# Kernel tuning notes

Measured on AMD Instinct MI355X. Metric: run time of the kernel, lower is better.

The kernel has to match this reference:

```python
import jax, jax.numpy as jnp
import numpy as np

N_TOKENS = 16384  # b * seq_len
D_MODEL = 4096
NUM_EXPERTS = 64
TOP_K = 2
EPS = 1e-8


def setup_inputs() -> dict:
    key = jax.random.key(0)
    kx, kw = jax.random.split(key)
    x = jax.random.normal(kx, (N_TOKENS, D_MODEL), dtype=jnp.float32)
    # nn.Linear weight: [num_experts, d_model], scaled like torch default init
    W = jax.random.normal(kw, (NUM_EXPERTS, D_MODEL), dtype=jnp.float32) / jnp.sqrt(D_MODEL)
    return {"x": x, "W": W}


def reference(x, W):
    # logits: [n_tokens, num_experts]
    logits = jnp.einsum('nd,ed->ne', x, W)
    scores = jax.nn.softmax(logits, axis=-1)
    topk_scores, topk_indices = jax.lax.top_k(scores, TOP_K)
    topk_scores = topk_scores / jnp.sum(topk_scores, axis=-1, keepdims=True)
    expert_prob = jnp.mean(scores, axis=0)  # [num_experts]
    load_balancing_loss = jnp.sum(expert_prob * jnp.log(expert_prob + EPS))
    return topk_scores, topk_indices, load_balancing_loss
```

## Files before the change

kernel.cpp:

```cpp
#include <hip/hip_runtime.h>
#include <hip/hip_bf16.h>

#define NT 16384
#define DM 4096
#define NE 64
#define MB 32
#define KSPLIT 4
#define KW (DM / KSPLIT)
#define KSTEPS (KW / 32)

typedef __attribute__((ext_vector_type(8))) short bf16x8;
typedef __attribute__((ext_vector_type(4))) float f32x4;

__device__ __forceinline__ unsigned short bf16_rne(float f) {
  const unsigned u = __float_as_uint(f);
  return (unsigned short)((u + 0x7FFFu + ((u >> 16) & 1u)) >> 16);
}

__device__ __forceinline__ void split2(float fa, float fb, unsigned& hp, unsigned& lp) {
  union { __hip_bfloat162 h; unsigned u; } cv;
  cv.h = __float22bfloat162_rn(make_float2(fa, fb));
  hp = cv.u;
  const float ha = __uint_as_float(hp << 16);
  const float hb = __uint_as_float(hp & 0xFFFF0000u);
  cv.h = __float22bfloat162_rn(make_float2(fa - ha, fb - hb));
  lp = cv.u;
}

__device__ __forceinline__ void splitA(const float4& c0, const float4& c1,
                                       bf16x8& hi, bf16x8& lo) {
  union { unsigned u[4]; bf16x8 v; } H, L;
  split2(c0.x, c0.y, H.u[0], L.u[0]);
  split2(c0.z, c0.w, H.u[1], L.u[1]);
  split2(c1.x, c1.y, H.u[2], L.u[2]);
  split2(c1.z, c1.w, H.u[3], L.u[3]);
  hi = H.v; lo = L.v;
}

__global__ void w_convert(const float* __restrict__ W,
                          unsigned short* __restrict__ Whi,
                          unsigned short* __restrict__ Wlo) {
  const int id   = blockIdx.x * 256 + threadIdx.x;
  const int lane = id & 63;
  const int nt   = (id >> 6) & 3;
  const int ks   = id >> 8;
  const float* src = W + (size_t)(nt * 16 + (lane & 15)) * DM + ks * 32 + (lane >> 4) * 8;
  unsigned short h[8], l[8];
#pragma unroll
  for (int j = 0; j < 8; ++j) {
    const float f = src[j];
    h[j] = bf16_rne(f);
    l[j] = bf16_rne(f - __uint_as_float((unsigned)h[j] << 16));
  }
  uint4 ph, pl;
  ph.x = h[0] | ((unsigned)h[1] << 16); ph.y = h[2] | ((unsigned)h[3] << 16);
  ph.z = h[4] | ((unsigned)h[5] << 16); ph.w = h[6] | ((unsigned)h[7] << 16);
  pl.x = l[0] | ((unsigned)l[1] << 16); pl.y = l[2] | ((unsigned)l[3] << 16);
  pl.z = l[4] | ((unsigned)l[5] << 16); pl.w = l[6] | ((unsigned)l[7] << 16);
  *(uint4*)(Whi + (size_t)id * 8) = ph;
  *(uint4*)(Wlo + (size_t)id * 8) = pl;
}

__launch_bounds__(256, 3)
__global__ void moe_mfma(const float* __restrict__ x,
                         const unsigned short* __restrict__ Whi,
                         const unsigned short* __restrict__ Wlo,
                         float* __restrict__ out,
                         float* __restrict__ bsum) {
  __shared__ float slab[KSPLIT][8][66];
  __shared__ float esums[4][NE];

  const int tid  = threadIdx.x;
  const int lane = tid & 63;
  const int wv   = tid >> 6;
  const int wvu  = __builtin_amdgcn_readfirstlane(wv);
  const int blk  = blockIdx.x;

  const float* ap0 = x + (size_t)(blk * MB + (lane & 15)) * DM + wv * KW + (lane >> 4) * 8;
  const float* ap1 = ap0 + (size_t)16 * DM;
  const unsigned short* bh_p = Whi + (size_t)(wv * KSTEPS) * 2048 + lane * 8;
  const unsigned short* bl_p = Wlo + (size_t)(wv * KSTEPS) * 2048 + lane * 8;

  f32x4 acc[2][4];
#pragma unroll
  for (int mt = 0; mt < 2; ++mt)
#pragma unroll
    for (int nt = 0; nt < 4; ++nt) acc[mt][nt] = (f32x4){0.f, 0.f, 0.f, 0.f};

  float4 a00 = *(const float4*)(ap0);
  float4 a01 = *(const float4*)(ap0 + 4);
  float4 a10 = *(const float4*)(ap1);
  float4 a11 = *(const float4*)(ap1 + 4);
  bf16x8 bh[4], bl[4];
#pragma unroll
  for (int nt = 0; nt < 4; ++nt) {
    bh[nt] = *(const bf16x8*)(bh_p + nt * 512);
    bl[nt] = *(const bf16x8*)(bl_p + nt * 512);
  }

#pragma unroll 2
  for (int i = 0; i < KSTEPS; ++i) {
    float4 p00, p01, p10, p11;
    bf16x8 nh[4], nl[4];
    if (i + 1 < KSTEPS) {
      const int o = (i + 1) * 32;
      p00 = *(const float4*)(ap0 + o);
      p01 = *(const float4*)(ap0 + o + 4);
      p10 = *(const float4*)(ap1 + o);
      p11 = *(const float4*)(ap1 + o + 4);
      const size_t fb = (size_t)(i + 1) * 2048;
#pragma unroll
      for (int nt = 0; nt < 4; ++nt) {
        nh[nt] = *(const bf16x8*)(bh_p + fb + nt * 512);
        nl[nt] = *(const bf16x8*)(bl_p + fb + nt * 512);
      }
    }

    bf16x8 ah0, al0, ah1, al1;
    splitA(a00, a01, ah0, al0);
    splitA(a10, a11, ah1, al1);

#pragma unroll
    for (int nt = 0; nt < 4; ++nt) {
      acc[0][nt] = __builtin_amdgcn_mfma_f32_16x16x32_bf16(al0, bl[nt], acc[0][nt], 0, 0, 0);
      acc[0][nt] = __builtin_amdgcn_mfma_f32_16x16x32_bf16(al0, bh[nt], acc[0][nt], 0, 0, 0);
      acc[0][nt] = __builtin_amdgcn_mfma_f32_16x16x32_bf16(ah0, bl[nt], acc[0][nt], 0, 0, 0);
      acc[0][nt] = __builtin_amdgcn_mfma_f32_16x16x32_bf16(ah0, bh[nt], acc[0][nt], 0, 0, 0);
      acc[1][nt] = __builtin_amdgcn_mfma_f32_16x16x32_bf16(al1, bl[nt], acc[1][nt], 0, 0, 0);
      acc[1][nt] = __builtin_amdgcn_mfma_f32_16x16x32_bf16(al1, bh[nt], acc[1][nt], 0, 0, 0);
      acc[1][nt] = __builtin_amdgcn_mfma_f32_16x16x32_bf16(ah1, bl[nt], acc[1][nt], 0, 0, 0);
      acc[1][nt] = __builtin_amdgcn_mfma_f32_16x16x32_bf16(ah1, bh[nt], acc[1][nt], 0, 0, 0);
    }

    if (i + 1 < KSTEPS) {
      a00 = p00; a01 = p01; a10 = p10; a11 = p11;
#pragma unroll
      for (int nt = 0; nt < 4; ++nt) { bh[nt] = nh[nt]; bl[nt] = nl[nt]; }
    }
  }

  float lg[8];
#pragma unroll
  for (int s = 0; s < 4; ++s) {
    const int mt = s >> 1;
    const int g  = 2 * (s & 1);
    const int q  = lane >> 4;
    if (q == g || q == g + 1) {
#pragma unroll
      for (int nt = 0; nt < 4; ++nt)
#pragma unroll
        for (int r = 0; r < 4; ++r)
          slab[wv][(q - g) * 4 + r][nt * 16 + (lane & 15)] = acc[mt][nt][r];
    }
    __syncthreads();
    if (wvu == s) {
#pragma unroll
      for (int t = 0; t < 8; ++t) {
        float v = 0.f;
#pragma unroll
        for (int w = 0; w < KSPLIT; ++w) v += slab[w][t][lane];
        lg[t] = v;
      }
    }
    __syncthreads();
  }

  float esum = 0.f;
#pragma unroll
  for (int ti = 0; ti < 8; ++ti) {
    const float lgv = lg[ti];
    float m = lgv;
#pragma unroll
    for (int off = 32; off; off >>= 1) m = fmaxf(m, __shfl_xor(m, off, 64));
    const float p = __expf(lgv - m);
    float Z = p;
#pragma unroll
    for (int off = 32; off; off >>= 1) Z += __shfl_xor(Z, off, 64);
    const float s = p / Z;
    esum += s;

    float v1 = s; int i1 = lane;
#pragma unroll
    for (int off = 32; off; off >>= 1) {
      const float ov = __shfl_xor(v1, off, 64);
      const int   oi = __shfl_xor(i1, off, 64);
      if (ov > v1 || (ov == v1 && oi < i1)) { v1 = ov; i1 = oi; }
    }
    float sv = (lane == i1) ? -1.f : s;
    float v2 = sv; int i2 = lane;
#pragma unroll
    for (int off = 32; off; off >>= 1) {
      const float ov = __shfl_xor(v2, off, 64);
      const int   oi = __shfl_xor(i2, off, 64);
      if (ov > v2 || (ov == v2 && oi < i2)) { v2 = ov; i2 = oi; }
    }

    if (lane == 0) {
      const int gt = blk * MB + wvu * 8 + ti;
      const float inv = 1.f / (v1 + v2);
      out[2 * gt]              = v1 * inv;
      out[2 * gt + 1]          = v2 * inv;
      out[2 * NT + 2 * gt]     = (float)i1;
      out[2 * NT + 2 * gt + 1] = (float)i2;
    }
  }

  esums[wvu][lane] = esum;
  __syncthreads();
  if (wvu == 0) {
    float tot = esums[0][lane] + esums[1][lane] + esums[2][lane] + esums[3][lane];
    bsum[blk * NE + lane] = tot;
  }
}

__global__ void moe_gate_loss(const float* __restrict__ bsum,
                              float* __restrict__ out) {
  __shared__ float red[4][64];
  const int e = threadIdx.x & 63;
  const int g = threadIdx.x >> 6;
  float s = 0.f;
  for (int b = g; b < NT / MB; b += 4) s += bsum[b * 64 + e];
  red[g][e] = s;
  __syncthreads();
  if (threadIdx.x < 64) {
    const float tot = red[0][e] + red[1][e] + red[2][e] + red[3][e];
    const float p = tot * (1.f / (float)NT);
    float term = p * logf(p + 1e-8f);
#pragma unroll
    for (int off = 32; off; off >>= 1) term += __shfl_xor(term, off, 64);
    if (e == 0) out[4 * NT] = term;
  }
}

extern "C" void kernel_launch(void* const* d_in, const int* in_sizes, int n_in,
                              void* d_out, int out_size, void* d_ws, size_t ws_size,
                              hipStream_t stream) {
  const float* x = (const float*)d_in[0];
  const float* W = (const float*)d_in[1];
  float* out = (float*)d_out;

  unsigned short* Whi = (unsigned short*)d_ws;
  unsigned short* Wlo = Whi + (size_t)NE * DM;
  float* bsum = (float*)(Wlo + (size_t)NE * DM);

  hipLaunchKernelGGL(w_convert, dim3(128), dim3(256), 0, stream, W, Whi, Wlo);
  hipLaunchKernelGGL(moe_mfma, dim3(NT / MB), dim3(256), 0, stream, x, Whi, Wlo, out, bsum);
  hipLaunchKernelGGL(moe_gate_loss, dim3(1), dim3(256), 0, stream, bsum, out);
}
```

Measured before the change: 111.2 us.

## Stage x tiles through double-buffered LDS and drop split-K reduction

The GEMM kernel now processes 64 tokens per block with 512 threads. Each wave owns a 16-token by 32-expert tile over the full K range, instead of four waves splitting K and reducing through shared memory. Activations are staged with coalesced row loads into a double-buffered LDS tile. Bf16 hi/lo weight fragments are software-pipelined from global memory. This removes the cross-wave split-K reduction and makes x loads coalesced, at the cost of a barrier per K stage and half the grid size.

```diff
diff --git a/kernel.cpp b/kernel.cpp
--- a/kernel.cpp
+++ b/kernel.cpp
@@ -4,10 +4,10 @@
 #define NT 16384
 #define DM 4096
 #define NE 64
-#define MB 32
-#define KSPLIT 4
-#define KW (DM / KSPLIT)
-#define KSTEPS (KW / 32)
+#define MB 64
+#define BK 128
+#define NST (DM / BK)
+#define LROW 132
 
 typedef __attribute__((ext_vector_type(8))) short bf16x8;
 typedef __attribute__((ext_vector_type(4))) float f32x4;
@@ -61,114 +61,107 @@
   *(uint4*)(Wlo + (size_t)id * 8) = pl;
 }
 
-__launch_bounds__(256, 3)
+__launch_bounds__(512, 2)
 __global__ void moe_mfma(const float* __restrict__ x,
                          const unsigned short* __restrict__ Whi,
                          const unsigned short* __restrict__ Wlo,
                          float* __restrict__ out,
                          float* __restrict__ bsum) {
-  __shared__ float slab[KSPLIT][8][66];
-  __shared__ float esums[4][NE];
+  __shared__ float xs[2][MB][LROW];
+  __shared__ float esums[8][NE];
+  float* lg = &xs[0][0][0];
 
   const int tid  = threadIdx.x;
   const int lane = tid & 63;
   const int wv   = tid >> 6;
   const int wvu  = __builtin_amdgcn_readfirstlane(wv);
+  const int tg   = wvu >> 1;
+  const int eg   = wvu & 1;
   const int blk  = blockIdx.x;
-
-  const float* ap0 = x + (size_t)(blk * MB + (lane & 15)) * DM + wv * KW + (lane >> 4) * 8;
-  const float* ap1 = ap0 + (size_t)16 * DM;
-  const unsigned short* bh_p = Whi + (size_t)(wv * KSTEPS) * 2048 + lane * 8;
-  const unsigned short* bl_p = Wlo + (size_t)(wv * KSTEPS) * 2048 + lane * 8;
-
-  f32x4 acc[2][4];
-#pragma unroll
-  for (int mt = 0; mt < 2; ++mt)
-#pragma unroll
-    for (int nt = 0; nt < 4; ++nt) acc[mt][nt] = (f32x4){0.f, 0.f, 0.f, 0.f};
-
-  float4 a00 = *(const float4*)(ap0);
-  float4 a01 = *(const float4*)(ap0 + 4);
-  float4 a10 = *(const float4*)(ap1);
-  float4 a11 = *(const float4*)(ap1 + 4);
-  bf16x8 bh[4], bl[4];
-#pragma unroll
-  for (int nt = 0; nt < 4; ++nt) {
-    bh[nt] = *(const bf16x8*)(bh_p + nt * 512);
-    bl[nt] = *(const bf16x8*)(bl_p + nt * 512);
-  }
-
-#pragma unroll 2
-  for (int i = 0; i < KSTEPS; ++i) {
-    float4 p00, p01, p10, p11;
-    bf16x8 nh[4], nl[4];
-    if (i + 1 < KSTEPS) {
-      const int o = (i + 1) * 32;
-      p00 = *(const float4*)(ap0 + o);
-      p01 = *(const float4*)(ap0 + o + 4);
-      p10 = *(const float4*)(ap1 + o);
-      p11 = *(const float4*)(ap1 + o + 4);
-      const size_t fb = (size_t)(i + 1) * 2048;
-#pragma unroll
-      for (int nt = 0; nt < 4; ++nt) {
-        nh[nt] = *(const bf16x8*)(bh_p + fb + nt * 512);
-        nl[nt] = *(const bf16x8*)(bl_p + fb + nt * 512);
-      }
-    }
-
-    bf16x8 ah0, al0, ah1, al1;
-    splitA(a00, a01, ah0, al0);
-    splitA(a10, a11, ah1, al1);
-
-#pragma unroll
-    for (int nt = 0; nt < 4; ++nt) {
-      acc[0][nt] = __builtin_amdgcn_mfma_f32_16x16x32_bf16(al0, bl[nt], acc[0][nt], 0, 0, 0);
-      acc[0][nt] = __builtin_amdgcn_mfma_f32_16x16x32_bf16(al0, bh[nt], acc[0][nt], 0, 0, 0);
-      acc[0][nt] = __builtin_amdgcn_mfma_f32_16x16x32_bf16(ah0, bl[nt], acc[0][nt], 0, 0, 0);
-      acc[0][nt] = __builtin_amdgcn_mfma_f32_16x16x32_bf16(ah0, bh[nt], acc[0][nt], 0, 0, 0);
-      acc[1][nt] = __builtin_amdgcn_mfma_f32_16x16x32_bf16(al1, bl[nt], acc[1][nt], 0, 0, 0);
-      acc[1][nt] = __builtin_amdgcn_mfma_f32_16x16x32_bf16(al1, bh[nt], acc[1][nt], 0, 0, 0);
-      acc[1][nt] = __builtin_amdgcn_mfma_f32_16x16x32_bf16(ah1, bl[nt], acc[1][nt], 0, 0, 0);
-      acc[1][nt] = __builtin_amdgcn_mfma_f32_16x16x32_bf16(ah1, bh[nt], acc[1][nt], 0, 0, 0);
-    }
-
-    if (i + 1 < KSTEPS) {
-      a00 = p00; a01 = p01; a10 = p10; a11 = p11;
-#pragma unroll
-      for (int nt = 0; nt < 4; ++nt) { bh[nt] = nh[nt]; bl[nt] = nl[nt]; }
-    }
-  }
-
-  float lg[8];
-#pragma unroll
-  for (int s = 0; s < 4; ++s) {
-    const int mt = s >> 1;
-    const int g  = 2 * (s & 1);
-    const int q  = lane >> 4;
-    if (q == g || q == g + 1) {
-#pragma unroll
-      for (int nt = 0; nt < 4; ++nt)
-#pragma unroll
-        for (int r = 0; r < 4; ++r)
-          slab[wv][(q - g) * 4 + r][nt * 16 + (lane & 15)] = acc[mt][nt][r];
-    }
+  const int tok0 = blk * MB;
+
+  const int srow = tid >> 3;
+  const int scol = (tid & 7) * 4;
+  const float* xrow = x + (size_t)(tok0 + srow) * DM + scol;
+
+  float4 g0, g1, g2, g3;
+#define LOADSTAGE(s) {                                        \
+    const float* p = xrow + (size_t)(s) * BK;                 \
+    g0 = *(const float4*)(p);                                 \
+    g1 = *(const float4*)(p + 32);                            \
+    g2 = *(const float4*)(p + 64);                            \
+    g3 = *(const float4*)(p + 96); }
+#define WRITESTAGE(b) {                                       \
+    float* q = &xs[b][srow][scol];                            \
+    *(float4*)(q)      = g0;                                  \
+    *(float4*)(q + 32) = g1;                                  \
+    *(float4*)(q + 64) = g2;                                  \
+    *(float4*)(q + 96) = g3; }
+
+  const unsigned short* bhp = Whi + (size_t)(eg * 2) * 512 + lane * 8;
+  const unsigned short* blp = Wlo + (size_t)(eg * 2) * 512 + lane * 8;
+  bf16x8 Bh0[2], Bl0[2], Bh1[2], Bl1[2];
+#define LOADB(BH, BL, gk) {                                   \
+    const size_t o = (size_t)(gk) * 2048;                     \
+    BH[0] = *(const bf16x8*)(bhp + o);                        \
+    BH[1] = *(const bf16x8*)(bhp + o + 512);                  \
+    BL[0] = *(const bf16x8*)(blp + o);                        \
+    BL[1] = *(const bf16x8*)(blp + o + 512); }
+
+  const int arow = tg * 16 + (lane & 15);
+  const int acol = (lane >> 4) * 8;
+
+  f32x4 acc0 = (f32x4){0.f, 0.f, 0.f, 0.f};
+  f32x4 acc1 = (f32x4){0.f, 0.f, 0.f, 0.f};
+
+#define STEP(b, kk, BH, BL) {                                                          \
+    const float* ap = &xs[b][arow][acol + (kk) * 32];                                  \
+    const float4 f0 = *(const float4*)(ap);                                            \
+    const float4 f1 = *(const float4*)(ap + 4);                                        \
+    bf16x8 ah, al;                                                                     \
+    splitA(f0, f1, ah, al);                                                            \
+    acc0 = __builtin_amdgcn_mfma_f32_16x16x32_bf16(al, BL[0], acc0, 0, 0, 0);          \
+    acc0 = __builtin_amdgcn_mfma_f32_16x16x32_bf16(al, BH[0], acc0, 0, 0, 0);          \
+    acc0 = __builtin_amdgcn_mfma_f32_16x16x32_bf16(ah, BL[0], acc0, 0, 0, 0);          \
+    acc0 = __builtin_amdgcn_mfma_f32_16x16x32_bf16(ah, BH[0], acc0, 0, 0, 0);          \
+    acc1 = __builtin_amdgcn_mfma_f32_16x16x32_bf16(al, BL[1], acc1, 0, 0, 0);          \
+    acc1 = __builtin_amdgcn_mfma_f32_16x16x32_bf16(al, BH[1], acc1, 0, 0, 0);          \
+    acc1 = __builtin_amdgcn_mfma_f32_16x16x32_bf16(ah, BL[1], acc1, 0, 0, 0);          \
+    acc1 = __builtin_amdgcn_mfma_f32_16x16x32_bf16(ah, BH[1], acc1, 0, 0, 0); }
+
+  LOADSTAGE(0);
+  LOADB(Bh0, Bl0, 0);
+  WRITESTAGE(0);
+  __syncthreads();
+
+  for (int s = 0; s < NST; ++s) {
+    const int b = s & 1;
+    if (s + 1 < NST) LOADSTAGE(s + 1);
+    const int g4 = s * 4;
+    const int n1 = g4 + 1, n2 = g4 + 2, n3 = g4 + 3;
+    const int n4 = (g4 + 4 < 128) ? g4 + 4 : 127;
+    LOADB(Bh1, Bl1, n1); STEP(b, 0, Bh0, Bl0);
+    LOADB(Bh0, Bl0, n2); STEP(b, 1, Bh1, Bl1);
+    LOADB(Bh1, Bl1, n3); STEP(b, 2, Bh0, Bl0);
+    LOADB(Bh0, Bl0, n4); STEP(b, 3, Bh1, Bl1);
+    if (s + 1 < NST) WRITESTAGE((s + 1) & 1);
     __syncthreads();
-    if (wvu == s) {
-#pragma unroll
-      for (int t = 0; t < 8; ++t) {
-        float v = 0.f;
-#pragma unroll
-        for (int w = 0; w < KSPLIT; ++w) v += slab[w][t][lane];
-        lg[t] = v;
-      }
-    }
-    __syncthreads();
-  }
+  }
+
+#pragma unroll
+  for (int r = 0; r < 4; ++r) {
+    const int t = tg * 16 + (lane >> 4) * 4 + r;
+    lg[t * 65 + eg * 32 + (lane & 15)]      = acc0[r];
+    lg[t * 65 + eg * 32 + 16 + (lane & 15)] = acc1[r];
+  }
+  __syncthreads();
 
   float esum = 0.f;
 #pragma unroll
   for (int ti = 0; ti < 8; ++ti) {
-    const float lgv = lg[ti];
+    const int t = wvu * 8 + ti;
+    const float lgv = lg[t * 65 + lane];
+
     float m = lgv;
 #pragma unroll
     for (int off = 32; off; off >>= 1) m = fmaxf(m, __shfl_xor(m, off, 64));
@@ -196,7 +189,7 @@
     }
 
     if (lane == 0) {
-      const int gt = blk * MB + wvu * 8 + ti;
+      const int gt = tok0 + t;
       const float inv = 1.f / (v1 + v2);
       out[2 * gt]              = v1 * inv;
       out[2 * gt + 1]          = v2 * inv;
@@ -208,7 +201,9 @@
   esums[wvu][lane] = esum;
   __syncthreads();
   if (wvu == 0) {
-    float tot = esums[0][lane] + esums[1][lane] + esums[2][lane] + esums[3][lane];
+    float tot = 0.f;
+#pragma unroll
+    for (int w = 0; w < 8; ++w) tot += esums[w][lane];
     bsum[blk * NE + lane] = tot;
   }
 }
@@ -244,6 +239,6 @@
   float* bsum = (float*)(Wlo + (size_t)NE * DM);
 
   hipLaunchKernelGGL(w_convert, dim3(128), dim3(256), 0, stream, W, Whi, Wlo);
-  hipLaunchKernelGGL(moe_mfma, dim3(NT / MB), dim3(256), 0, stream, x, Whi, Wlo, out, bsum);
+  hipLaunchKernelGGL(moe_mfma, dim3(NT / MB), dim3(512), 0, stream, x, Whi, Wlo, out, bsum);
   hipLaunchKernelGGL(moe_gate_loss, dim3(1), dim3(256), 0, stream, bsum, out);
 }
```

After: 106.0 us. 4.6% less time.
